# Kernel optimization log

Measured on AMD Instinct MI355X. Metric: run time of the kernel, lower is better.

## Reference

```python
import jax, jax.numpy as jnp
import numpy as np

B, S, H, E, I = 2, 1024, 1024, 8, 512
EPS = 1e-8  # torch F.cosine_similarity eps


def setup_inputs() -> dict:
    key = jax.random.key(0)
    ks = jax.random.split(key, 5)
    return {
        "hidden_states": jax.random.normal(ks[0], (B, S, H), dtype=jnp.float32),
        "expert_embeddings": jax.random.normal(ks[1], (E, H), dtype=jnp.float32),
        # torch init is zeros; -0.03 keeps the zero-selection fallback (which NaNs the
        # original's softmax) from ever triggering while preserving ~half-dense routing
        "gate_threshold": jnp.full((E,), -0.03, dtype=jnp.float32),
        "w_gate": jax.random.normal(ks[2], (E, H, I), dtype=jnp.float32) / np.sqrt(H).astype(np.float32),
        "w_up": jax.random.normal(ks[3], (E, H, I), dtype=jnp.float32) / np.sqrt(H).astype(np.float32),
        "w_down": jax.random.normal(ks[4], (E, I, H), dtype=jnp.float32) / np.sqrt(I).astype(np.float32),
    }


def _forward(hidden_states, expert_embeddings, gate_threshold, w_gate, w_up, w_down):
    b, s, h = hidden_states.shape
    n_experts = expert_embeddings.shape[0]
    x = hidden_states.reshape(-1, h)  # [T, H]

    # cosine-similarity routing scores [T, E]
    xn = x / jnp.maximum(jnp.linalg.norm(x, axis=-1, keepdims=True), EPS)
    en = expert_embeddings / jnp.maximum(jnp.linalg.norm(expert_embeddings, axis=-1, keepdims=True), EPS)
    scores = xn @ en.T

    # SiLUHardThreshold forward: hard 0/1 mask (used only as a boolean downstream,
    # so no gradient flows through it in the module's output path)
    routing_mask = (jax.nn.silu(scores - gate_threshold) > 0).astype(scores.dtype)

    # guarantee at least one expert per token: fall back to top-1 score
    num_sel = routing_mask.sum(axis=-1)  # [T]
    top1 = jnp.argmax(scores, axis=-1)   # [T]
    routing_mask_final = jnp.where((num_sel == 0)[:, None],
                                   jax.nn.one_hot(top1, n_experts, dtype=scores.dtype),
                                   routing_mask)

    # softmax over selected experts (pre-fallback mask, as in the original)
    masked_scores = jnp.where(routing_mask > 0, scores, -jnp.inf)
    routing_weights = jax.nn.softmax(masked_scores.astype(jnp.float32), axis=-1).astype(x.dtype)
    gates = routing_weights * routing_mask_final  # [T, E] combine weights

    # per-expert Qwen3 SwiGLU MLP: down(silu(gate(x)) * up(x)); dense over experts,
    # gated combine is the vectorized equivalent of the gather/MLP/index_add loop
    hmid = jax.nn.silu(jnp.einsum('th,ehi->eti', x, w_gate)) * jnp.einsum('th,ehi->eti', x, w_up)  # [E,T,I]
    out = jnp.einsum('eti,eih,te->th', hmid, w_down, gates)  # [T, H]

    return out.reshape(b, s, h), scores


def reference(hidden_states, expert_embeddings, gate_threshold, w_gate, w_up, w_down):
    # returns (final_hidden_states [B,S,H], router_logits [T,E])
    return _forward(hidden_states, expert_embeddings, gate_threshold, w_gate, w_up, w_down)
```

## Files before the change

kernel.cpp:

```cpp
#include <hip/hip_runtime.h>
#include <hip/hip_bf16.h>
#include <stdint.h>

#define T_TOK 2048
#define H_DIM 1024
#define E_NUM 8
#define I_DIM 512
#define KDOWN (E_NUM * I_DIM)
#define EPSR 1e-8f

typedef short s16x8 __attribute__((ext_vector_type(8)));
typedef float f32x4 __attribute__((ext_vector_type(4)));

static __device__ __forceinline__ uint16_t f2bf(float f) {
    union { float f; uint32_t i; } v; v.f = f;
    uint32_t lsb = (v.i >> 16) & 1u;
    v.i += 0x7fffu + lsb;
    return (uint16_t)(v.i >> 16);
}

static __device__ __forceinline__ void gll16(const void* g, void* l) {
    __builtin_amdgcn_global_load_lds(
        (const __attribute__((address_space(1))) void*)g,
        (__attribute__((address_space(3))) void*)l, 16, 0, 0);
}

__global__ __launch_bounds__(256) void prep_kernel(
    const float* __restrict__ wg, const float* __restrict__ wu,
    const float* __restrict__ wd, uint16_t* __restrict__ wB,
    uint16_t* __restrict__ wdT,
    const float* __restrict__ x, const float* __restrict__ emb,
    const float* __restrict__ thr, float* __restrict__ scores_out,
    float* __restrict__ gates, uint16_t* __restrict__ xb) {
    __shared__ union {
        float tile[64][68];
        struct { float semb[E_NUM * H_DIM]; float senorm[E_NUM]; } r;
    } sm;
    const int bid = blockIdx.x;
    const int tid = threadIdx.x;

    if (bid < 3072) {
        const int bz = bid >> 7, by = (bid >> 3) & 15, bx = bid & 7;
        const int g16 = tid >> 4, l16 = (tid & 15) * 4;
        if (bz < 16) {
            const int e = bz & 7;
            const int isU = (bz >= 8);
            const float* src = (isU ? wu : wg) + (long)e * H_DIM * I_DIM;
            const int r0 = by * 64, c0 = bx * 64;
            #pragma unroll
            for (int it = 0; it < 4; ++it) {
                int r = it * 16 + g16;
                *(float4*)&sm.tile[r][l16] = *(const float4*)(src + (long)(r0 + r) * I_DIM + c0 + l16);
            }
            __syncthreads();
            #pragma unroll
            for (int it = 0; it < 4; ++it) {
                int oc = it * 16 + g16;
                int i = c0 + oc;
                ushort4 o;
                o.x = f2bf(sm.tile[l16 + 0][oc]);
                o.y = f2bf(sm.tile[l16 + 1][oc]);
                o.z = f2bf(sm.tile[l16 + 2][oc]);
                o.w = f2bf(sm.tile[l16 + 3][oc]);
                long rbig = ((long)e << 10) + ((i >> 4) << 5) + (isU << 4) + (i & 15);
                *(ushort4*)(wB + rbig * H_DIM + r0 + l16) = o;
            }
        } else {
            const int e = bz - 16;
            const float* src = wd + (long)e * I_DIM * H_DIM;
            uint16_t* dst = wdT + (long)e * I_DIM;
            const int r0 = bx * 64, c0 = by * 64;
            #pragma unroll
            for (int it = 0; it < 4; ++it) {
                int r = it * 16 + g16;
                *(float4*)&sm.tile[r][l16] = *(const float4*)(src + (long)(r0 + r) * H_DIM + c0 + l16);
            }
            __syncthreads();
            #pragma unroll
            for (int it = 0; it < 4; ++it) {
                int oc = it * 16 + g16;
                ushort4 o;
                o.x = f2bf(sm.tile[l16 + 0][oc]);
                o.y = f2bf(sm.tile[l16 + 1][oc]);
                o.z = f2bf(sm.tile[l16 + 2][oc]);
                o.w = f2bf(sm.tile[l16 + 3][oc]);
                *(ushort4*)(dst + (long)(c0 + oc) * KDOWN + r0 + l16) = o;
            }
        }
        return;
    }
    const int rb = bid - 3072;
    const int lane = tid & 63;
    const int wave = tid >> 6;
    for (int i = tid; i < E_NUM * H_DIM; i += 256) sm.r.semb[i] = emb[i];
    __syncthreads();
    for (int e = wave; e < E_NUM; e += 4) {
        float s = 0.f;
        #pragma unroll
        for (int c = 0; c < 16; ++c) { float v = sm.r.semb[e * H_DIM + lane + 64 * c]; s += v * v; }
        #pragma unroll
        for (int off = 32; off; off >>= 1) s += __shfl_xor(s, off);
        if (lane == 0) sm.r.senorm[e] = fmaxf(sqrtf(s), EPSR);
    }
    __syncthreads();
    const int t = rb * 4 + wave;
    const float* xt = x + (long)t * H_DIM;
    uint16_t* xbt = xb + (long)t * H_DIM;
    float nrm = 0.f, dot[E_NUM];
    #pragma unroll
    for (int e = 0; e < E_NUM; ++e) dot[e] = 0.f;
    #pragma unroll
    for (int c = 0; c < 16; ++c) {
        float v = xt[lane + 64 * c];
        xbt[lane + 64 * c] = f2bf(v);
        nrm += v * v;
        #pragma unroll
        for (int e = 0; e < E_NUM; ++e) dot[e] += v * sm.r.semb[e * H_DIM + lane + 64 * c];
    }
    #pragma unroll
    for (int off = 32; off; off >>= 1) {
        nrm += __shfl_xor(nrm, off);
        #pragma unroll
        for (int e = 0; e < E_NUM; ++e) dot[e] += __shfl_xor(dot[e], off);
    }
    float xn = fmaxf(sqrtf(nrm), EPSR);
    float sc[E_NUM], sel[E_NUM];
    float msel = -1e30f, mall = -1e30f;
    int nsel = 0, arg = 0;
    #pragma unroll
    for (int e = 0; e < E_NUM; ++e) {
        sc[e] = dot[e] / (xn * sm.r.senorm[e]);
        float d = sc[e] - thr[e];
        sel[e] = (d > 0.f) ? 1.f : 0.f;
        if (d > 0.f) { nsel++; msel = fmaxf(msel, sc[e]); }
        if (sc[e] > mall) { mall = sc[e]; arg = e; }
    }
    float w[E_NUM], den = 0.f;
    #pragma unroll
    for (int e = 0; e < E_NUM; ++e) { w[e] = (sel[e] > 0.f) ? __expf(sc[e] - msel) : 0.f; den += w[e]; }
    if (lane == 0) {
        #pragma unroll
        for (int e = 0; e < E_NUM; ++e) {
            scores_out[t * E_NUM + e] = sc[e];
            gates[t * E_NUM + e] = (nsel > 0) ? (w[e] / den) : ((e == arg) ? 1.f : 0.f);
        }
    }
}

__global__ __launch_bounds__(512, 2) void moe_gateup_kernel(
    const uint16_t* __restrict__ xb,
    const uint16_t* __restrict__ wB,
    const float* __restrict__ gates,
    uint16_t* __restrict__ hmid) {
    const int bid = blockIdx.x;
    const int xcd = bid & 7, j = bid >> 3;
    const int by = xcd * 4 + (j >> 3);
    const int bx = j & 7;
    const int t0 = bx * 256;
    const int n0 = by * 256;
    const int e  = by >> 2;

    __shared__ uint16_t sA[4][256][32];
    __shared__ uint16_t sB[4][256][32];
    __shared__ float sGate[256];

    const int tid  = threadIdx.x;
    const int lane = tid & 63;
    const int wave = tid >> 6;
    const int wm = wave >> 2, wn = wave & 3;

    if (tid < 256) sGate[tid] = gates[(t0 + tid) * E_NUM + e];
    __syncthreads();

    const int lr = lane >> 2;
    const int cl = ((lane & 3) ^ ((lane >> 3) & 3)) * 8;
    const uint16_t* gA = xb + (long)(t0 + wave * 16 + lr) * H_DIM + cl;
    const uint16_t* gB = wB + (long)(n0 + wave * 16 + lr) * H_DIM + cl;

#define STA(sl, kt) do { \
        gll16(gA + (long)(kt) * 32,                &sA[sl][wave * 16][0]); \
        gll16(gA + 128L * H_DIM + (long)(kt) * 32, &sA[sl][128 + wave * 16][0]); } while (0)
#define STB(sl, kt) do { \
        gll16(gB + (long)(kt) * 32,                &sB[sl][wave * 16][0]); \
        gll16(gB + 128L * H_DIM + (long)(kt) * 32, &sB[sl][128 + wave * 16][0]); } while (0)

    const int q = lane >> 4, r16 = lane & 15;
    const int pc = (q ^ ((r16 >> 1) & 3)) * 8;

    f32x4 acc[8][4] = {};

    STA(0, 0); STB(0, 0);
    STA(1, 1); STB(1, 1);
    STA(2, 2); STB(2, 2);
    asm volatile("s_waitcnt vmcnt(8)" ::: "memory");
    __builtin_amdgcn_s_barrier();
    asm volatile("" ::: "memory");

    #pragma unroll 1
    for (int s = 0; s < 32; ++s) {
        const int sl = s & 3;
        s16x8 af[8], bf[4];
        #pragma unroll
        for (int m = 0; m < 8; ++m)
            af[m] = *(const s16x8*)&sA[sl][wm * 128 + m * 16 + r16][pc];
        bf[0] = *(const s16x8*)&sB[sl][wn * 64 + 0 * 16 + r16][pc];
        bf[1] = *(const s16x8*)&sB[sl][wn * 64 + 1 * 16 + r16][pc];
        if (s + 3 < 32) STA((s + 3) & 3, s + 3);
        asm volatile("" ::: "memory");
        __builtin_amdgcn_s_barrier();
        asm volatile("" ::: "memory");
        __builtin_amdgcn_s_setprio(1);
        #pragma unroll
        for (int m = 0; m < 8; ++m) {
            acc[m][0] = __builtin_amdgcn_mfma_f32_16x16x32_bf16(af[m], bf[0], acc[m][0], 0, 0, 0);
            acc[m][1] = __builtin_amdgcn_mfma_f32_16x16x32_bf16(af[m], bf[1], acc[m][1], 0, 0, 0);
        }
        __builtin_amdgcn_s_setprio(0);
        asm volatile("" ::: "memory");
        __builtin_amdgcn_s_barrier();
        asm volatile("" ::: "memory");
        bf[2] = *(const s16x8*)&sB[sl][wn * 64 + 2 * 16 + r16][pc];
        bf[3] = *(const s16x8*)&sB[sl][wn * 64 + 3 * 16 + r16][pc];
        if (s + 3 < 32) STB((s + 3) & 3, s + 3);
        if (s < 29)      asm volatile("s_waitcnt vmcnt(8)" ::: "memory");
        else if (s == 29) asm volatile("s_waitcnt vmcnt(4)" ::: "memory");
        else             asm volatile("s_waitcnt vmcnt(0)" ::: "memory");
        __builtin_amdgcn_s_barrier();
        asm volatile("" ::: "memory");
        __builtin_amdgcn_s_setprio(1);
        #pragma unroll
        for (int m = 0; m < 8; ++m) {
            acc[m][2] = __builtin_amdgcn_mfma_f32_16x16x32_bf16(af[m], bf[2], acc[m][2], 0, 0, 0);
            acc[m][3] = __builtin_amdgcn_mfma_f32_16x16x32_bf16(af[m], bf[3], acc[m][3], 0, 0, 0);
        }
        __builtin_amdgcn_s_setprio(0);
        asm volatile("" ::: "memory");
        __builtin_amdgcn_s_barrier();
        asm volatile("" ::: "memory");
    }
#undef STA
#undef STB

    #pragma unroll
    for (int m = 0; m < 8; ++m) {
        #pragma unroll
        for (int rr = 0; rr < 4; ++rr) {
            const int trow = wm * 128 + m * 16 + q * 4 + rr;
            const float gate = sGate[trow];
            const long tglob = t0 + trow;
            #pragma unroll
            for (int p = 0; p < 2; ++p) {
                float g = acc[m][2 * p][rr], u = acc[m][2 * p + 1][rr];
                float h = gate * (g / (1.f + __expf(-g))) * u;
                const int cb = n0 + wn * 64 + p * 32;
                const int i = (((cb & 1023) >> 5) << 4) + r16;
                hmid[tglob * KDOWN + e * I_DIM + i] = f2bf(h);
            }
        }
    }
}

__global__ __launch_bounds__(256, 3) void moe_down_kernel(
    const uint16_t* __restrict__ hmid,
    const uint16_t* __restrict__ wdT,
    float* __restrict__ out,
    float* __restrict__ parts) {
    const int bid = blockIdx.x + 8 * (blockIdx.y + 16 * blockIdx.z);
    const int r  = bid & 7;
    const int j  = bid >> 3;
    const int h0 = ((r & 1) * 4 + (j & 3)) * 128;
    const int t0 = ((r >> 1) * 4 + ((j >> 2) & 3)) * 128;
    const int kz = j >> 4;
    const int kst = kz * 1024;
    __shared__ uint16_t sA[128][64];
    __shared__ uint16_t sB[128][64];
    const int tid  = threadIdx.x;
    const int lane = tid & 63;
    const int wave = tid >> 6;
    const int wm = wave >> 1, wn = wave & 1;

    const int srow = wave * 32 + (lane >> 3);
    const int scol = ((lane & 7) ^ (srow & 7)) * 8;
    const uint16_t* ga = hmid + (long)(t0 + srow) * KDOWN + scol;
    const uint16_t* gb = wdT  + (long)(h0 + srow) * KDOWN + scol;

    f32x4 acc[4][4] = {};
    const int q = lane >> 4, r16 = lane & 15;
    const int sw = r16 & 7;

    for (int kb = kst; kb < kst + 1024; kb += 64) {
        __syncthreads();
        #pragma unroll
        for (int j2 = 0; j2 < 4; ++j2) {
            const int lr = wave * 32 + j2 * 8;
            gll16(ga + (long)j2 * 8 * KDOWN + kb, &sA[lr][0]);
            gll16(gb + (long)j2 * 8 * KDOWN + kb, &sB[lr][0]);
        }
        __syncthreads();
        #pragma unroll
        for (int kk = 0; kk < 2; ++kk) {
            const int pc = ((kk * 4 + q) ^ sw) * 8;
            s16x8 af[4], bf[4];
            #pragma unroll
            for (int m = 0; m < 4; ++m)
                af[m] = *(const s16x8*)&sA[wm * 64 + m * 16 + r16][pc];
            #pragma unroll
            for (int n = 0; n < 4; ++n)
                bf[n] = *(const s16x8*)&sB[wn * 64 + n * 16 + r16][pc];
            #pragma unroll
            for (int m = 0; m < 4; ++m)
                #pragma unroll
                for (int n = 0; n < 4; ++n)
                    acc[m][n] = __builtin_amdgcn_mfma_f32_16x16x32_bf16(af[m], bf[n], acc[m][n], 0, 0, 0);
        }
    }
    float* dst = (kz == 0) ? out : (parts + (long)(kz - 1) * T_TOK * H_DIM);
    #pragma unroll
    for (int m = 0; m < 4; ++m) {
        #pragma unroll
        for (int rr = 0; rr < 4; ++rr) {
            const int t = t0 + wm * 64 + m * 16 + q * 4 + rr;
            #pragma unroll
            for (int n = 0; n < 4; ++n)
                dst[(long)t * H_DIM + h0 + wn * 64 + n * 16 + r16] = acc[m][n][rr];
        }
    }
}

__global__ __launch_bounds__(256) void reduce_kernel(float* __restrict__ out,
                                                     const float* __restrict__ parts) {
    long i = ((long)blockIdx.x * 256 + threadIdx.x) * 4;
    float4 a = *(const float4*)(out + i);
    #pragma unroll
    for (int j = 0; j < 3; ++j) {
        float4 b = *(const float4*)(parts + (long)j * T_TOK * H_DIM + i);
        a.x += b.x; a.y += b.y; a.z += b.z; a.w += b.w;
    }
    *(float4*)(out + i) = a;
}

extern "C" void kernel_launch(void* const* d_in, const int* in_sizes, int n_in,
                              void* d_out, int out_size, void* d_ws, size_t ws_size,
                              hipStream_t stream) {
    const float* x    = (const float*)d_in[0];
    const float* emb  = (const float*)d_in[1];
    const float* thr  = (const float*)d_in[2];
    const float* wg   = (const float*)d_in[3];
    const float* wu   = (const float*)d_in[4];
    const float* wd   = (const float*)d_in[5];
    float* out    = (float*)d_out;
    float* scores = out + (size_t)T_TOK * H_DIM;

    uint8_t* ws = (uint8_t*)d_ws;
    uint16_t* xb   = (uint16_t*)(ws);
    uint16_t* wB   = (uint16_t*)(ws + (size_t)4  * 1048576);
    uint16_t* wdT  = (uint16_t*)(ws + (size_t)20 * 1048576);
    uint16_t* hmid = (uint16_t*)(ws + (size_t)28 * 1048576);
    float*    gates = (float*)  (ws + (size_t)44 * 1048576);
    float*    parts = (float*)  (ws + (size_t)48 * 1048576);

    prep_kernel<<<3072 + T_TOK / 4, 256, 0, stream>>>(
        wg, wu, wd, wB, wdT, x, emb, thr, scores, gates, xb);
    moe_gateup_kernel<<<256, 512, 0, stream>>>(xb, wB, gates, hmid);
    moe_down_kernel<<<dim3(H_DIM / 128, T_TOK / 128, 4), 256, 0, stream>>>(hmid, wdT, out, parts);
    reduce_kernel<<<(T_TOK * H_DIM) / 1024, 256, 0, stream>>>(out, parts);
}
```

Baseline: 173.5 us.

## Simplify gate-up pipeline to one barrier per step and multi-buffer down GEMM

The gate/up GEMM main loop drops its split two-phase schedule, which used three barriers per k-step, in favour of one wait-and-barrier at the top of each step. It then issues the next stage's A and B loads together and runs all 32 MFMAs at once. The down-projection kernel moves from a single-buffered 64-wide k tile with two __syncthreads per step to a 4-stage ring of 32-wide k tiles, prefetched three steps ahead with the same vmcnt-based waits. Its launch bounds drop from 3 to 2 blocks per SM to allow for the extra LDS and registers. The aim is to cut barrier overhead and hide global-load latency in both GEMMs, at the cost of lower occupancy in the down kernel.

```diff
diff --git a/kernel.cpp b/kernel.cpp
--- a/kernel.cpp
+++ b/kernel.cpp
@@ -192,51 +192,30 @@
     STA(0, 0); STB(0, 0);
     STA(1, 1); STB(1, 1);
     STA(2, 2); STB(2, 2);
-    asm volatile("s_waitcnt vmcnt(8)" ::: "memory");
-    __builtin_amdgcn_s_barrier();
-    asm volatile("" ::: "memory");
 
     #pragma unroll 1
     for (int s = 0; s < 32; ++s) {
         const int sl = s & 3;
+        if (s < 30)       asm volatile("s_waitcnt vmcnt(8)" ::: "memory");
+        else if (s == 30) asm volatile("s_waitcnt vmcnt(4)" ::: "memory");
+        else              asm volatile("s_waitcnt vmcnt(0)" ::: "memory");
+        __builtin_amdgcn_s_barrier();
+        asm volatile("" ::: "memory");
+        if (s + 3 < 32) { STA((s + 3) & 3, s + 3); STB((s + 3) & 3, s + 3); }
         s16x8 af[8], bf[4];
         #pragma unroll
         for (int m = 0; m < 8; ++m)
             af[m] = *(const s16x8*)&sA[sl][wm * 128 + m * 16 + r16][pc];
-        bf[0] = *(const s16x8*)&sB[sl][wn * 64 + 0 * 16 + r16][pc];
-        bf[1] = *(const s16x8*)&sB[sl][wn * 64 + 1 * 16 + r16][pc];
-        if (s + 3 < 32) STA((s + 3) & 3, s + 3);
-        asm volatile("" ::: "memory");
-        __builtin_amdgcn_s_barrier();
-        asm volatile("" ::: "memory");
+        #pragma unroll
+        for (int n = 0; n < 4; ++n)
+            bf[n] = *(const s16x8*)&sB[sl][wn * 64 + n * 16 + r16][pc];
         __builtin_amdgcn_s_setprio(1);
         #pragma unroll
-        for (int m = 0; m < 8; ++m) {
-            acc[m][0] = __builtin_amdgcn_mfma_f32_16x16x32_bf16(af[m], bf[0], acc[m][0], 0, 0, 0);
-            acc[m][1] = __builtin_amdgcn_mfma_f32_16x16x32_bf16(af[m], bf[1], acc[m][1], 0, 0, 0);
-        }
+        for (int m = 0; m < 8; ++m)
+            #pragma unroll
+            for (int n = 0; n < 4; ++n)
+                acc[m][n] = __builtin_amdgcn_mfma_f32_16x16x32_bf16(af[m], bf[n], acc[m][n], 0, 0, 0);
         __builtin_amdgcn_s_setprio(0);
-        asm volatile("" ::: "memory");
-        __builtin_amdgcn_s_barrier();
-        asm volatile("" ::: "memory");
-        bf[2] = *(const s16x8*)&sB[sl][wn * 64 + 2 * 16 + r16][pc];
-        bf[3] = *(const s16x8*)&sB[sl][wn * 64 + 3 * 16 + r16][pc];
-        if (s + 3 < 32) STB((s + 3) & 3, s + 3);
-        if (s < 29)      asm volatile("s_waitcnt vmcnt(8)" ::: "memory");
-        else if (s == 29) asm volatile("s_waitcnt vmcnt(4)" ::: "memory");
-        else             asm volatile("s_waitcnt vmcnt(0)" ::: "memory");
-        __builtin_amdgcn_s_barrier();
-        asm volatile("" ::: "memory");
-        __builtin_amdgcn_s_setprio(1);
-        #pragma unroll
-        for (int m = 0; m < 8; ++m) {
-            acc[m][2] = __builtin_amdgcn_mfma_f32_16x16x32_bf16(af[m], bf[2], acc[m][2], 0, 0, 0);
-            acc[m][3] = __builtin_amdgcn_mfma_f32_16x16x32_bf16(af[m], bf[3], acc[m][3], 0, 0, 0);
-        }
-        __builtin_amdgcn_s_setprio(0);
-        asm volatile("" ::: "memory");
-        __builtin_amdgcn_s_barrier();
-        asm volatile("" ::: "memory");
     }
 #undef STA
 #undef STB
@@ -260,7 +239,7 @@
     }
 }
 
-__global__ __launch_bounds__(256, 3) void moe_down_kernel(
+__global__ __launch_bounds__(256, 2) void moe_down_kernel(
     const uint16_t* __restrict__ hmid,
     const uint16_t* __restrict__ wdT,
     float* __restrict__ out,
@@ -272,48 +251,60 @@
     const int t0 = ((r >> 1) * 4 + ((j >> 2) & 3)) * 128;
     const int kz = j >> 4;
     const int kst = kz * 1024;
-    __shared__ uint16_t sA[128][64];
-    __shared__ uint16_t sB[128][64];
+    __shared__ uint16_t sA[4][128][32];
+    __shared__ uint16_t sB[4][128][32];
     const int tid  = threadIdx.x;
     const int lane = tid & 63;
     const int wave = tid >> 6;
     const int wm = wave >> 1, wn = wave & 1;
 
-    const int srow = wave * 32 + (lane >> 3);
-    const int scol = ((lane & 7) ^ (srow & 7)) * 8;
-    const uint16_t* ga = hmid + (long)(t0 + srow) * KDOWN + scol;
-    const uint16_t* gb = wdT  + (long)(h0 + srow) * KDOWN + scol;
+    const int lr = lane >> 2;
+    const int cl = ((lane & 3) ^ ((lane >> 3) & 3)) * 8;
+    const uint16_t* gA = hmid + (long)(t0 + wave * 32 + lr) * KDOWN + kst + cl;
+    const uint16_t* gB = wdT  + (long)(h0 + wave * 32 + lr) * KDOWN + kst + cl;
+
+#define STA(sl, kt) do { \
+        gll16(gA + (long)(kt) * 32,               &sA[sl][wave * 32][0]); \
+        gll16(gA + 16L * KDOWN + (long)(kt) * 32, &sA[sl][wave * 32 + 16][0]); } while (0)
+#define STB(sl, kt) do { \
+        gll16(gB + (long)(kt) * 32,               &sB[sl][wave * 32][0]); \
+        gll16(gB + 16L * KDOWN + (long)(kt) * 32, &sB[sl][wave * 32 + 16][0]); } while (0)
 
     f32x4 acc[4][4] = {};
     const int q = lane >> 4, r16 = lane & 15;
-    const int sw = r16 & 7;
-
-    for (int kb = kst; kb < kst + 1024; kb += 64) {
-        __syncthreads();
-        #pragma unroll
-        for (int j2 = 0; j2 < 4; ++j2) {
-            const int lr = wave * 32 + j2 * 8;
-            gll16(ga + (long)j2 * 8 * KDOWN + kb, &sA[lr][0]);
-            gll16(gb + (long)j2 * 8 * KDOWN + kb, &sB[lr][0]);
-        }
-        __syncthreads();
-        #pragma unroll
-        for (int kk = 0; kk < 2; ++kk) {
-            const int pc = ((kk * 4 + q) ^ sw) * 8;
-            s16x8 af[4], bf[4];
-            #pragma unroll
-            for (int m = 0; m < 4; ++m)
-                af[m] = *(const s16x8*)&sA[wm * 64 + m * 16 + r16][pc];
+    const int pc = (q ^ ((r16 >> 1) & 3)) * 8;
+
+    STA(0, 0); STB(0, 0);
+    STA(1, 1); STB(1, 1);
+    STA(2, 2); STB(2, 2);
+
+    #pragma unroll 1
+    for (int s = 0; s < 32; ++s) {
+        const int sl = s & 3;
+        if (s < 30)       asm volatile("s_waitcnt vmcnt(8)" ::: "memory");
+        else if (s == 30) asm volatile("s_waitcnt vmcnt(4)" ::: "memory");
+        else              asm volatile("s_waitcnt vmcnt(0)" ::: "memory");
+        __builtin_amdgcn_s_barrier();
+        asm volatile("" ::: "memory");
+        if (s + 3 < 32) { STA((s + 3) & 3, s + 3); STB((s + 3) & 3, s + 3); }
+        s16x8 af[4], bf[4];
+        #pragma unroll
+        for (int m = 0; m < 4; ++m)
+            af[m] = *(const s16x8*)&sA[sl][wm * 64 + m * 16 + r16][pc];
+        #pragma unroll
+        for (int n = 0; n < 4; ++n)
+            bf[n] = *(const s16x8*)&sB[sl][wn * 64 + n * 16 + r16][pc];
+        __builtin_amdgcn_s_setprio(1);
+        #pragma unroll
+        for (int m = 0; m < 4; ++m)
             #pragma unroll
             for (int n = 0; n < 4; ++n)
-                bf[n] = *(const s16x8*)&sB[wn * 64 + n * 16 + r16][pc];
-            #pragma unroll
-            for (int m = 0; m < 4; ++m)
-                #pragma unroll
-                for (int n = 0; n < 4; ++n)
-                    acc[m][n] = __builtin_amdgcn_mfma_f32_16x16x32_bf16(af[m], bf[n], acc[m][n], 0, 0, 0);
-        }
-    }
+                acc[m][n] = __builtin_amdgcn_mfma_f32_16x16x32_bf16(af[m], bf[n], acc[m][n], 0, 0, 0);
+        __builtin_amdgcn_s_setprio(0);
+    }
+#undef STA
+#undef STB
+
     float* dst = (kz == 0) ? out : (parts + (long)(kz - 1) * T_TOK * H_DIM);
     #pragma unroll
     for (int m = 0; m < 4; ++m) {
```

New measurement: 187.6 us. 8.1% more time.
